# Kernel tuning notes

Measured on AMD Instinct MI355X. Metric: run time of the kernel, lower is better.

The kernel has to match this reference:

```python
import jax, jax.numpy as jnp
import numpy as np

WIN = (8, 8, 8)
NUM_HEADS = 8
DIM = 256


def _make_rel_tables(win):
    Wh, Ww, Wd = win
    # relative coords table, matching the torch buffer construction
    ch = np.arange(-(Wh - 1), Wh, dtype=np.float32)
    cw = np.arange(-(Ww - 1), Ww, dtype=np.float32)
    cd = np.arange(-(Wd - 1), Wd, dtype=np.float32)
    g = np.stack(np.meshgrid(ch, cw, cd, indexing='ij'), axis=-1)  # (2Wh-1,2Ww-1,2Wd-1,3)
    g[..., 0] /= (Wh - 1)
    g[..., 1] /= (Ww - 1)
    g[..., 2] /= (Wd - 1)
    g *= 8.0
    g = np.sign(g) * np.log2(np.abs(g) + 1.0) / np.log2(8.0)
    table = g.reshape(-1, 3).astype(np.float32)  # (3375, 3)
    # relative position index (meshgrid order coords_d, coords_h, coords_w as in source)
    ah = np.arange(Wh)
    aw = np.arange(Ww)
    ad = np.arange(Wd)
    coords = np.stack(np.meshgrid(ad, ah, aw, indexing='ij'))  # (3, Wd, Wh, Ww)
    cf = coords.reshape(3, -1)  # (3, N)
    rel = cf[:, :, None] - cf[:, None, :]  # (3, N, N)
    rel = rel.transpose(1, 2, 0).astype(np.int64)
    rel[:, :, 0] += Wh - 1
    rel[:, :, 1] += Ww - 1
    rel[:, :, 2] += Wd - 1
    rel[:, :, 0] *= (2 * Ww - 1) * (2 * Wd - 1)
    rel[:, :, 1] *= 2 * Wd - 1
    idx = rel.sum(-1).astype(np.int32)  # (N, N)
    return jnp.asarray(table), jnp.asarray(idx)


def setup_inputs() -> dict:
    key = jax.random.key(0)
    ks = jax.random.split(key, 8)
    B_, N, C, nH = 128, 512, DIM, NUM_HEADS
    table, idx = _make_rel_tables(WIN)
    return {
        'x': jax.random.normal(ks[0], (B_, N, C), jnp.float32),
        'mask': jnp.zeros((64, N, N), jnp.float32),
        'qkv_w': jax.random.normal(ks[1], (3 * C, C), jnp.float32) * 0.02,
        'q_bias': jnp.zeros((C,), jnp.float32),
        'v_bias': jnp.zeros((C,), jnp.float32),
        'logit_scale': jnp.log(10.0 * jnp.ones((nH, 1, 1), jnp.float32)),
        'cpb_w1': jax.random.normal(ks[2], (512, 3), jnp.float32) * 0.1,
        'cpb_b1': jnp.zeros((512,), jnp.float32),
        'cpb_w2': jax.random.normal(ks[3], (nH, 512), jnp.float32) * 0.05,
        'proj_w': jax.random.normal(ks[4], (C, C), jnp.float32) * 0.02,
        'proj_b': jnp.zeros((C,), jnp.float32),
        'rel_coords_table': table,
        'rel_pos_index': idx,
    }


def reference(x, mask, qkv_w, q_bias, v_bias, logit_scale, cpb_w1, cpb_b1,
              cpb_w2, proj_w, proj_b, rel_coords_table, rel_pos_index):
    B_, N, C = x.shape
    nH = NUM_HEADS
    d = C // nH
    # qkv projection with (q_bias, 0, v_bias) bias
    qkv_bias = jnp.concatenate([q_bias, jnp.zeros_like(v_bias), v_bias])
    qkv = x @ qkv_w.T + qkv_bias  # (B_, N, 3C)
    qkv = qkv.reshape(B_, N, 3, nH, d).transpose(2, 0, 3, 1, 4)  # (3, B_, nH, N, d)
    q, k, v = qkv[0], qkv[1], qkv[2]
    # cosine attention: L2-normalize q and k along head dim (eps as in F.normalize)
    qn = q / jnp.maximum(jnp.linalg.norm(q, axis=-1, keepdims=True), 1e-12)
    kn = k / jnp.maximum(jnp.linalg.norm(k, axis=-1, keepdims=True), 1e-12)
    attn = jnp.einsum('bhnd,bhmd->bhnm', qn, kn)  # (B_, nH, N, N)
    scale = jnp.exp(jnp.minimum(logit_scale, jnp.log(100.0)))  # clamp at log(1/0.01)
    attn = attn * scale[None]  # (nH,1,1) broadcast
    # MLP-computed relative position bias
    hdn = jax.nn.relu(rel_coords_table @ cpb_w1.T + cpb_b1)  # (T, 512)
    bias_table = hdn @ cpb_w2.T  # (T, nH)
    rpb = bias_table[rel_pos_index]  # (N, N, nH)
    rpb = 16.0 * jax.nn.sigmoid(rpb.transpose(2, 0, 1))  # (nH, N, N)
    attn = attn + rpb[None]
    # mask add (0 / -inf per-window mask)
    nW = mask.shape[0]
    attn = attn.reshape(B_ // nW, nW, nH, N, N) + mask[None, :, None]
    attn = attn.reshape(B_, nH, N, N)
    attn = jax.nn.softmax(attn, axis=-1)
    out = jnp.einsum('bhnm,bhmd->bhnd', attn, v)
    out = out.transpose(0, 2, 1, 3).reshape(B_, N, C)
    return out @ proj_w.T + proj_b
```

## Files before the change

### kernel.cpp

```cpp
#include <hip/hip_runtime.h>
#include <cstddef>
#include <cstdint>
#include <math.h>

#define NB   128
#define SEQ  512
#define CH   256
#define NH   8
#define HD   32
#define TBL  3375
#define LOG100 4.6051701859880914f

typedef _Float16 f16x8 __attribute__((ext_vector_type(8)));
typedef _Float16 f16x4 __attribute__((ext_vector_type(4)));
typedef float    f32x4 __attribute__((ext_vector_type(4)));

__device__ inline f32x4 mfma16(f16x8 a, f16x8 b, f32x4 c) {
    return __builtin_amdgcn_mfma_f32_16x16x32_f16(a, b, c, 0, 0, 0);
}

__device__ inline unsigned short h2b(_Float16 h) {
    union { _Float16 f; unsigned short s; } u; u.f = h; return u.s;
}

__global__ __launch_bounds__(256)
void split_inplace(unsigned int* buf, int rows)
{
    int wid = (blockIdx.x << 2) + (threadIdx.x >> 6);
    int ln  = threadIdx.x & 63;
    if (wid >= rows) return;
    unsigned int* row = buf + (size_t)wid * 256;
    uint4 u = ((const uint4*)row)[ln];
    float x0 = __uint_as_float(u.x), x1 = __uint_as_float(u.y),
          x2 = __uint_as_float(u.z), x3 = __uint_as_float(u.w);
    _Float16 hh0 = (_Float16)x0, hh1 = (_Float16)x1,
             hh2 = (_Float16)x2, hh3 = (_Float16)x3;
    _Float16 ll0 = (_Float16)(x0 - (float)hh0), ll1 = (_Float16)(x1 - (float)hh1),
             ll2 = (_Float16)(x2 - (float)hh2), ll3 = (_Float16)(x3 - (float)hh3);
    unsigned int hi01 = (unsigned int)h2b(hh0) | ((unsigned int)h2b(hh1) << 16);
    unsigned int hi23 = (unsigned int)h2b(hh2) | ((unsigned int)h2b(hh3) << 16);
    unsigned int lo01 = (unsigned int)h2b(ll0) | ((unsigned int)h2b(ll1) << 16);
    unsigned int lo23 = (unsigned int)h2b(ll2) | ((unsigned int)h2b(ll3) << 16);
    asm volatile("" ::: "memory");
    *(uint2*)(row + 2 * ln)       = make_uint2(hi01, hi23);
    *(uint2*)(row + 128 + 2 * ln) = make_uint2(lo01, lo23);
}

template<int EPI>
__global__ __launch_bounds__(256)
void mgemm(const _Float16* __restrict__ A, const _Float16* __restrict__ W,
           float* __restrict__ qb, float* __restrict__ kb, float* __restrict__ vb,
           const float* __restrict__ q_bias, const float* __restrict__ v_bias,
           const float* __restrict__ logit_scale,
           float* __restrict__ out, const float* __restrict__ obias)
{
    __shared__ alignas(16) _Float16 As[128 * 64];
    __shared__ alignas(16) _Float16 Bs[128 * 64];
    const int t  = threadIdx.x;
    const int ln = t & 63;
    const int wv = t >> 6;
    const int wr = wv >> 1, wc = wv & 1;
    const int m0 = blockIdx.x * 128, n0 = blockIdx.y * 128;

    f32x4 acc[4][4];
#pragma unroll
    for (int i = 0; i < 4; ++i)
#pragma unroll
        for (int j = 0; j < 4; ++j) acc[i][j] = (f32x4){0.f, 0.f, 0.f, 0.f};

    for (int step = 0; step < 12; ++step) {
        const int term = step >> 2;
        const int k0   = (step & 3) * 64;
        const int aoff = (term == 2) ? 256 : 0;
        const int woff = (term == 1) ? 256 : 0;
        if (step) __syncthreads();
#pragma unroll
        for (int u = 0; u < 4; ++u) {
            int f = u * 256 + t;
            int r = f >> 3, s = f & 7;
            int sw = s ^ (r & 7);
            uint4 av = *(const uint4*)(A + (size_t)(m0 + r) * 512 + aoff + k0 + s * 8);
            *(uint4*)(As + r * 64 + sw * 8) = av;
            uint4 wv4 = *(const uint4*)(W + (size_t)(n0 + r) * 512 + woff + k0 + s * 8);
            *(uint4*)(Bs + r * 64 + sw * 8) = wv4;
        }
        __syncthreads();
#pragma unroll
        for (int kh = 0; kh < 2; ++kh) {
            const int g = kh * 4 + (ln >> 4);
            f16x8 af[4], bf[4];
#pragma unroll
            for (int fm = 0; fm < 4; ++fm) {
                int r = wr * 64 + fm * 16 + (ln & 15);
                af[fm] = *(const f16x8*)(As + r * 64 + (g ^ (r & 7)) * 8);
            }
#pragma unroll
            for (int fn = 0; fn < 4; ++fn) {
                int r = wc * 64 + fn * 16 + (ln & 15);
                bf[fn] = *(const f16x8*)(Bs + r * 64 + (g ^ (r & 7)) * 8);
            }
#pragma unroll
            for (int fm = 0; fm < 4; ++fm)
#pragma unroll
                for (int fn = 0; fn < 4; ++fn)
                    acc[fm][fn] = mfma16(af[fm], bf[fn], acc[fm][fn]);
        }
    }

    if (EPI == 0) {
#pragma unroll
        for (int fm = 0; fm < 4; ++fm) {
#pragma unroll
            for (int fn = 0; fn < 4; ++fn) {
                int col = n0 + wc * 64 + fn * 16 + (ln & 15);
                float bv = obias[col];
#pragma unroll
                for (int r = 0; r < 4; ++r) {
                    int m = m0 + wr * 64 + fm * 16 + (ln >> 4) * 4 + r;
                    out[(size_t)m * CH + col] = acc[fm][fn][r] + bv;
                }
            }
        }
    } else {
        const int cbase = n0 + wc * 64;
        const int which = cbase >> 8;
#pragma unroll
        for (int fp = 0; fp < 2; ++fp) {
            const int c0  = cbase + fp * 32;
            const int rem = c0 & 255;
            const int h   = rem >> 5;
            float bias0 = 0.f, bias1 = 0.f;
            if (which == 0) {
                bias0 = q_bias[rem + (ln & 15)];
                bias1 = q_bias[rem + 16 + (ln & 15)];
            } else if (which == 2) {
                bias0 = v_bias[rem + (ln & 15)];
                bias1 = v_bias[rem + 16 + (ln & 15)];
            }
            float scl = 1.f;
            if (which == 0) scl = __expf(fminf(logit_scale[h], LOG100));
            float* dst = (which == 0) ? qb : (which == 1 ? kb : vb);
#pragma unroll
            for (int fm = 0; fm < 4; ++fm) {
#pragma unroll
                for (int r = 0; r < 4; ++r) {
                    float v0 = acc[fm][fp * 2][r]     + bias0;
                    float v1 = acc[fm][fp * 2 + 1][r] + bias1;
                    if (which < 2) {
                        float ss = v0 * v0 + v1 * v1;
#pragma unroll
                        for (int mk = 1; mk < 16; mk <<= 1)
                            ss += __shfl_xor(ss, mk, 64);
                        float mult = 1.f / fmaxf(sqrtf(ss), 1e-12f);
                        if (which == 0) mult *= scl;
                        v0 *= mult; v1 *= mult;
                    }
                    int m = m0 + wr * 64 + fm * 16 + (ln >> 4) * 4 + r;
                    int b = m >> 9, nseq = m & 511;
                    size_t base = (((size_t)b * NH + h) * SEQ + nseq) * HD;
                    dst[base + (ln & 15)]      = v0;
                    dst[base + 16 + (ln & 15)] = v1;
                }
            }
        }
    }
}

__global__ __launch_bounds__(256)
void cpb_kernel(const float* __restrict__ tbl, const float* __restrict__ w1,
                const float* __restrict__ b1, const float* __restrict__ w2,
                float* __restrict__ bt)
{
    __shared__ alignas(16) float red[256][8];
    int t = blockIdx.x;
    float c0 = tbl[t*3+0], c1 = tbl[t*3+1], c2 = tbl[t*3+2];
    float part[8] = {0,0,0,0,0,0,0,0};
    for (int j = threadIdx.x; j < 512; j += 256) {
        float h = c0*w1[j*3+0] + c1*w1[j*3+1] + c2*w1[j*3+2] + b1[j];
        h = fmaxf(h, 0.f);
#pragma unroll
        for (int o = 0; o < 8; ++o) part[o] += h * w2[o*512 + j];
    }
#pragma unroll
    for (int o = 0; o < 8; ++o) red[threadIdx.x][o] = part[o];
    __syncthreads();
    for (int s = 128; s >= 1; s >>= 1) {
        if (threadIdx.x < s)
#pragma unroll
            for (int o = 0; o < 8; ++o) red[threadIdx.x][o] += red[threadIdx.x + s][o];
        __syncthreads();
    }
    if (threadIdx.x < 8) bt[t*8 + threadIdx.x] = red[0][threadIdx.x];
}

__global__ __launch_bounds__(256)
void rpb_kernel(const int* __restrict__ idx, const float* __restrict__ bt,
                float* __restrict__ rpb)
{
    int h = blockIdx.x >> 9;
    int i = blockIdx.x & 511;
    for (int j = threadIdx.x; j < 512; j += 256) {
        int id = idx[i*512 + j];
        float x = bt[id*8 + h];
        rpb[((size_t)h*512 + i)*512 + j] = 16.f / (1.f + __expf(-x));
    }
}

__global__ __launch_bounds__(256)
void attn_kernel(const float* __restrict__ qn, const float* __restrict__ kn,
                 const float* __restrict__ vv, const float* __restrict__ rpb,
                 const float* __restrict__ mask, _Float16* __restrict__ ao16)
{
    __shared__ alignas(16) float Ks[64][32];
    __shared__ alignas(16) float Vs[64][32];
    const int b = blockIdx.x >> 3, h = blockIdx.x & 7;
    const int n0 = threadIdx.x, n1 = threadIdx.x + 256;

    const float* qrow0 = qn + (((size_t)b*NH + h)*SEQ + n0)*HD;
    const float* qrow1 = qn + (((size_t)b*NH + h)*SEQ + n1)*HD;
    float4 qa[8], qc[8];
#pragma unroll
    for (int i = 0; i < 8; ++i) { qa[i] = ((const float4*)qrow0)[i];
                                  qc[i] = ((const float4*)qrow1)[i]; }

    float4 Oa[8], Oc[8];
#pragma unroll
    for (int i = 0; i < 8; ++i) { Oa[i] = make_float4(0,0,0,0);
                                  Oc[i] = make_float4(0,0,0,0); }
    float la = 0.f, lc = 0.f;

    const float* kbase = kn + ((size_t)b*NH + h)*SEQ*HD;
    const float* vbase = vv + ((size_t)b*NH + h)*SEQ*HD;
    const float* rr0 = rpb  + ((size_t)h*SEQ + n0)*SEQ;
    const float* rr1 = rpb  + ((size_t)h*SEQ + n1)*SEQ;
    const float* mr0 = mask + ((size_t)(b & 63)*SEQ + n0)*SEQ;
    const float* mr1 = mask + ((size_t)(b & 63)*SEQ + n1)*SEQ;

    for (int kt = 0; kt < 8; ++kt) {
        if (kt) __syncthreads();
        const float4* ksrc = (const float4*)(kbase + kt*64*32);
        const float4* vsrc = (const float4*)(vbase + kt*64*32);
        float4* kd = (float4*)&Ks[0][0];
        float4* vd = (float4*)&Vs[0][0];
        kd[threadIdx.x]       = ksrc[threadIdx.x];
        kd[threadIdx.x + 256] = ksrc[threadIdx.x + 256];
        vd[threadIdx.x]       = vsrc[threadIdx.x];
        vd[threadIdx.x + 256] = vsrc[threadIdx.x + 256];
        __syncthreads();

#pragma unroll 1
        for (int jc = 0; jc < 16; ++jc) {
            const int j0 = jc * 4;
            float4 ra = *(const float4*)(rr0 + kt*64 + j0);
            float4 rc = *(const float4*)(rr1 + kt*64 + j0);
            float4 ma = *(const float4*)(mr0 + kt*64 + j0);
            float4 mc = *(const float4*)(mr1 + kt*64 + j0);
            float ba[4] = {ra.x+ma.x, ra.y+ma.y, ra.z+ma.z, ra.w+ma.w};
            float bc[4] = {rc.x+mc.x, rc.y+mc.y, rc.z+mc.z, rc.w+mc.w};
#pragma unroll
            for (int jj = 0; jj < 4; ++jj) {
                const int j = j0 + jj;
                const float4* kr = (const float4*)&Ks[j][0];
                float d0 = 0.f, d1 = 0.f;
#pragma unroll
                for (int dq = 0; dq < 8; ++dq) {
                    float4 kq = kr[dq];
                    d0 += qa[dq].x*kq.x + qa[dq].y*kq.y + qa[dq].z*kq.z + qa[dq].w*kq.w;
                    d1 += qc[dq].x*kq.x + qc[dq].y*kq.y + qc[dq].z*kq.z + qc[dq].w*kq.w;
                }
                float p0 = __expf(d0 + ba[jj]);
                float p1 = __expf(d1 + bc[jj]);
                la += p0; lc += p1;
                const float4* vr = (const float4*)&Vs[j][0];
#pragma unroll
                for (int dq = 0; dq < 8; ++dq) {
                    float4 vq = vr[dq];
                    Oa[dq].x += p0*vq.x; Oa[dq].y += p0*vq.y;
                    Oa[dq].z += p0*vq.z; Oa[dq].w += p0*vq.w;
                    Oc[dq].x += p1*vq.x; Oc[dq].y += p1*vq.y;
                    Oc[dq].z += p1*vq.z; Oc[dq].w += p1*vq.w;
                }
            }
        }
    }

    float ia = 1.f / la, ic = 1.f / lc;
    _Float16* o0 = ao16 + ((size_t)(b*SEQ + n0))*512 + h*HD;
    _Float16* o1 = ao16 + ((size_t)(b*SEQ + n1))*512 + h*HD;
#pragma unroll
    for (int dq = 0; dq < 8; ++dq) {
        float r0[4] = {Oa[dq].x*ia, Oa[dq].y*ia, Oa[dq].z*ia, Oa[dq].w*ia};
        float r1[4] = {Oc[dq].x*ic, Oc[dq].y*ic, Oc[dq].z*ic, Oc[dq].w*ic};
        f16x4 h0, l0, h1, l1;
#pragma unroll
        for (int e = 0; e < 4; ++e) {
            _Float16 hh = (_Float16)r0[e];
            h0[e] = hh; l0[e] = (_Float16)(r0[e] - (float)hh);
            _Float16 hg = (_Float16)r1[e];
            h1[e] = hg; l1[e] = (_Float16)(r1[e] - (float)hg);
        }
        *(f16x4*)(o0 + dq*4)       = h0;
        *(f16x4*)(o0 + 256 + dq*4) = l0;
        *(f16x4*)(o1 + dq*4)       = h1;
        *(f16x4*)(o1 + 256 + dq*4) = l1;
    }
}

extern "C" void kernel_launch(void* const* d_in, const int* in_sizes, int n_in,
                              void* d_out, int out_size, void* d_ws, size_t ws_size,
                              hipStream_t stream)
{
    float* x           = (float*)d_in[0];
    const float* mask        = (const float*)d_in[1];
    float* qkv_w       = (float*)d_in[2];
    const float* q_bias      = (const float*)d_in[3];
    const float* v_bias      = (const float*)d_in[4];
    const float* logit_scale = (const float*)d_in[5];
    const float* cpb_w1      = (const float*)d_in[6];
    const float* cpb_b1      = (const float*)d_in[7];
    const float* cpb_w2      = (const float*)d_in[8];
    float* proj_w      = (float*)d_in[9];
    const float* proj_b      = (const float*)d_in[10];
    const float* tblc        = (const float*)d_in[11];
    const int*   rpidx       = (const int*)d_in[12];

    float* ws = (float*)d_ws;
    const size_t SZ = (size_t)NB * SEQ * CH;
    float* qb     = ws;
    float* kb     = qb + SZ;
    float* vb     = kb + SZ;
    float* rpbbuf = vb + SZ;
    float* bt     = rpbbuf + (size_t)NH * SEQ * SEQ;

    split_inplace<<<16384, 256, 0, stream>>>((unsigned int*)x, NB * SEQ);
    split_inplace<<<192, 256, 0, stream>>>((unsigned int*)qkv_w, 3 * CH);
    split_inplace<<<64, 256, 0, stream>>>((unsigned int*)proj_w, CH);
    mgemm<1><<<dim3(512, 6), dim3(256), 0, stream>>>(
        (const _Float16*)x, (const _Float16*)qkv_w,
        qb, kb, vb, q_bias, v_bias, logit_scale, nullptr, nullptr);
    cpb_kernel<<<TBL, 256, 0, stream>>>(tblc, cpb_w1, cpb_b1, cpb_w2, bt);
    rpb_kernel<<<NH * SEQ, 256, 0, stream>>>(rpidx, bt, rpbbuf);
    attn_kernel<<<NB * NH, 256, 0, stream>>>(qb, kb, vb, rpbbuf, mask,
                                             (_Float16*)x);
    mgemm<0><<<dim3(512, 2), dim3(256), 0, stream>>>(
        (const _Float16*)x, (const _Float16*)proj_w,
        nullptr, nullptr, nullptr, nullptr, nullptr, nullptr,
        (float*)d_out, proj_b);
}
```

Measured before the change: 1.169 ms.

## Move attention to MFMA with split-fp16 Q/K/V, transposed V, and mask-skip flag

Replaces the scalar fp32 attention loop with an MFMA-based flash-attention kernel. It uses hi/lo fp16 splits for Q, K, V and P to keep near-fp32 accuracy, and an online softmax with P staged in shared memory. The QKV GEMM epilogue now writes split fp16 rows, and a new transpose kernel lays V out for the PV product. A scan kernel sets a flag when the mask has any nonzero entry, so mask loads can be skipped when it is all zero. The grid grows to one block per 64-query tile, adding parallelism. In exchange it adds extra kernel launches, a full pass over the mask, and reuse of the output buffer as scratch.

```diff
diff --git a/kernel.cpp b/kernel.cpp
--- a/kernel.cpp
+++ b/kernel.cpp
@@ -49,7 +49,8 @@
 template<int EPI>
 __global__ __launch_bounds__(256)
 void mgemm(const _Float16* __restrict__ A, const _Float16* __restrict__ W,
-           float* __restrict__ qb, float* __restrict__ kb, float* __restrict__ vb,
+           _Float16* __restrict__ qb16, _Float16* __restrict__ kb16,
+           _Float16* __restrict__ vstr16,
            const float* __restrict__ q_bias, const float* __restrict__ v_bias,
            const float* __restrict__ logit_scale,
            float* __restrict__ out, const float* __restrict__ obias)
@@ -139,7 +140,8 @@
             }
             float scl = 1.f;
             if (which == 0) scl = __expf(fminf(logit_scale[h], LOG100));
-            float* dst = (which == 0) ? qb : (which == 1 ? kb : vb);
+            _Float16* dst = (which == 0) ? qb16 : (which == 1 ? kb16 : vstr16);
+            const int dd = ln & 15;
 #pragma unroll
             for (int fm = 0; fm < 4; ++fm) {
 #pragma unroll
@@ -157,12 +159,57 @@
                     }
                     int m = m0 + wr * 64 + fm * 16 + (ln >> 4) * 4 + r;
                     int b = m >> 9, nseq = m & 511;
-                    size_t base = (((size_t)b * NH + h) * SEQ + nseq) * HD;
-                    dst[base + (ln & 15)]      = v0;
-                    dst[base + 16 + (ln & 15)] = v1;
+                    size_t rowb = (((size_t)b * NH + h) * SEQ + nseq) * 64;
+                    _Float16 h0 = (_Float16)v0, h1 = (_Float16)v1;
+                    _Float16 l0 = (_Float16)(v0 - (float)h0);
+                    _Float16 l1 = (_Float16)(v1 - (float)h1);
+                    dst[rowb + dd]           = h0;
+                    dst[rowb + 16 + dd]      = h1;
+                    dst[rowb + 32 + dd]      = l0;
+                    dst[rowb + 48 + dd]      = l1;
                 }
             }
         }
+    }
+}
+
+__global__ __launch_bounds__(256)
+void vtrans(const _Float16* __restrict__ vs, _Float16* __restrict__ vt)
+{
+    __shared__ alignas(16) _Float16 T[64][136];
+    const int bh = blockIdx.x, t = threadIdx.x;
+    const _Float16* src = vs + (size_t)bh * 32768;
+    _Float16* dst = vt + (size_t)bh * 32768;
+    for (int tile = 0; tile < 4; ++tile) {
+        if (tile) __syncthreads();
+        const int n = (t >> 1);
+        const int sbase = (t & 1) * 32;
+        const uint4* sp = (const uint4*)(src + ((size_t)(tile * 128 + n)) * 64 + sbase);
+#pragma unroll
+        for (int q = 0; q < 4; ++q) {
+            uint4 u = sp[q];
+            _Float16 tmp[8];
+            *(uint4*)tmp = u;
+#pragma unroll
+            for (int e = 0; e < 8; ++e)
+                T[sbase + q * 8 + e][n] = tmp[e];
+        }
+        __syncthreads();
+        const int cc = t >> 2, nn = (t & 3) * 32;
+        uint4* dp = (uint4*)(dst + (size_t)cc * 512 + tile * 128 + nn);
+        const uint4* lp = (const uint4*)(&T[cc][nn]);
+        dp[0] = lp[0]; dp[1] = lp[1]; dp[2] = lp[2]; dp[3] = lp[3];
+    }
+}
+
+__global__ __launch_bounds__(256)
+void maskflag(const unsigned int* __restrict__ mask, unsigned int* flag, int n)
+{
+    unsigned int acc = 0;
+    for (int i = blockIdx.x * 256 + threadIdx.x; i < n; i += gridDim.x * 256)
+        acc |= mask[i];
+    if (__ballot(acc != 0)) {
+        if ((threadIdx.x & 63) == 0) atomicOr(flag, 1u);
     }
 }
 
@@ -206,103 +253,133 @@
     }
 }
 
-__global__ __launch_bounds__(256)
-void attn_kernel(const float* __restrict__ qn, const float* __restrict__ kn,
-                 const float* __restrict__ vv, const float* __restrict__ rpb,
-                 const float* __restrict__ mask, _Float16* __restrict__ ao16)
-{
-    __shared__ alignas(16) float Ks[64][32];
-    __shared__ alignas(16) float Vs[64][32];
-    const int b = blockIdx.x >> 3, h = blockIdx.x & 7;
-    const int n0 = threadIdx.x, n1 = threadIdx.x + 256;
-
-    const float* qrow0 = qn + (((size_t)b*NH + h)*SEQ + n0)*HD;
-    const float* qrow1 = qn + (((size_t)b*NH + h)*SEQ + n1)*HD;
-    float4 qa[8], qc[8];
-#pragma unroll
-    for (int i = 0; i < 8; ++i) { qa[i] = ((const float4*)qrow0)[i];
-                                  qc[i] = ((const float4*)qrow1)[i]; }
-
-    float4 Oa[8], Oc[8];
-#pragma unroll
-    for (int i = 0; i < 8; ++i) { Oa[i] = make_float4(0,0,0,0);
-                                  Oc[i] = make_float4(0,0,0,0); }
-    float la = 0.f, lc = 0.f;
-
-    const float* kbase = kn + ((size_t)b*NH + h)*SEQ*HD;
-    const float* vbase = vv + ((size_t)b*NH + h)*SEQ*HD;
-    const float* rr0 = rpb  + ((size_t)h*SEQ + n0)*SEQ;
-    const float* rr1 = rpb  + ((size_t)h*SEQ + n1)*SEQ;
-    const float* mr0 = mask + ((size_t)(b & 63)*SEQ + n0)*SEQ;
-    const float* mr1 = mask + ((size_t)(b & 63)*SEQ + n1)*SEQ;
+__global__ __launch_bounds__(256, 4)
+void attn_kernel(const _Float16* __restrict__ qb, const _Float16* __restrict__ kb,
+                 const _Float16* __restrict__ vbt, const float* __restrict__ rpb,
+                 const float* __restrict__ mask, const unsigned int* __restrict__ mflag,
+                 _Float16* __restrict__ ao16)
+{
+    __shared__ float Pl[4][16][68];
+    const int idx = blockIdx.x;
+    const int h  = idx & 7;
+    const int qt = (idx >> 3) & 7;
+    const int b  = idx >> 6;
+    const int w  = threadIdx.x >> 6;
+    const int ln = threadIdx.x & 63;
+    const int c  = ln & 15, g = ln >> 4;
+    const int q0 = qt * 64 + w * 16;
+    const size_t bh = (size_t)b * NH + h;
+
+    const _Float16* qrow = qb + (bh * SEQ + q0) * 64;
+    f16x8 qh = *(const f16x8*)(qrow + (size_t)c * 64 + g * 8);
+    f16x8 qlo = *(const f16x8*)(qrow + (size_t)c * 64 + 32 + g * 8);
+
+    const _Float16* kbase = kb + bh * SEQ * 64;
+    const _Float16* vtb   = vbt + bh * 32768;
+    const float* rbase = rpb  + ((size_t)h * SEQ + q0) * SEQ;
+    const float* mbase = mask + ((size_t)(b & 63) * SEQ + q0) * SEQ;
+    const bool usemask = (*mflag) != 0u;
+
+    f32x4 O0 = {0,0,0,0}, O1 = {0,0,0,0};
+    float mrun[4] = {-INFINITY, -INFINITY, -INFINITY, -INFINITY};
+    float lr[4] = {0.f, 0.f, 0.f, 0.f};
 
     for (int kt = 0; kt < 8; ++kt) {
-        if (kt) __syncthreads();
-        const float4* ksrc = (const float4*)(kbase + kt*64*32);
-        const float4* vsrc = (const float4*)(vbase + kt*64*32);
-        float4* kd = (float4*)&Ks[0][0];
-        float4* vd = (float4*)&Vs[0][0];
-        kd[threadIdx.x]       = ksrc[threadIdx.x];
-        kd[threadIdx.x + 256] = ksrc[threadIdx.x + 256];
-        vd[threadIdx.x]       = vsrc[threadIdx.x];
-        vd[threadIdx.x + 256] = vsrc[threadIdx.x + 256];
-        __syncthreads();
-
-#pragma unroll 1
-        for (int jc = 0; jc < 16; ++jc) {
-            const int j0 = jc * 4;
-            float4 ra = *(const float4*)(rr0 + kt*64 + j0);
-            float4 rc = *(const float4*)(rr1 + kt*64 + j0);
-            float4 ma = *(const float4*)(mr0 + kt*64 + j0);
-            float4 mc = *(const float4*)(mr1 + kt*64 + j0);
-            float ba[4] = {ra.x+ma.x, ra.y+ma.y, ra.z+ma.z, ra.w+ma.w};
-            float bc[4] = {rc.x+mc.x, rc.y+mc.y, rc.z+mc.z, rc.w+mc.w};
-#pragma unroll
-            for (int jj = 0; jj < 4; ++jj) {
-                const int j = j0 + jj;
-                const float4* kr = (const float4*)&Ks[j][0];
-                float d0 = 0.f, d1 = 0.f;
-#pragma unroll
-                for (int dq = 0; dq < 8; ++dq) {
-                    float4 kq = kr[dq];
-                    d0 += qa[dq].x*kq.x + qa[dq].y*kq.y + qa[dq].z*kq.z + qa[dq].w*kq.w;
-                    d1 += qc[dq].x*kq.x + qc[dq].y*kq.y + qc[dq].z*kq.z + qc[dq].w*kq.w;
-                }
-                float p0 = __expf(d0 + ba[jj]);
-                float p1 = __expf(d1 + bc[jj]);
-                la += p0; lc += p1;
-                const float4* vr = (const float4*)&Vs[j][0];
-#pragma unroll
-                for (int dq = 0; dq < 8; ++dq) {
-                    float4 vq = vr[dq];
-                    Oa[dq].x += p0*vq.x; Oa[dq].y += p0*vq.y;
-                    Oa[dq].z += p0*vq.z; Oa[dq].w += p0*vq.w;
-                    Oc[dq].x += p1*vq.x; Oc[dq].y += p1*vq.y;
-                    Oc[dq].z += p1*vq.z; Oc[dq].w += p1*vq.w;
-                }
-            }
-        }
-    }
-
-    float ia = 1.f / la, ic = 1.f / lc;
-    _Float16* o0 = ao16 + ((size_t)(b*SEQ + n0))*512 + h*HD;
-    _Float16* o1 = ao16 + ((size_t)(b*SEQ + n1))*512 + h*HD;
-#pragma unroll
-    for (int dq = 0; dq < 8; ++dq) {
-        float r0[4] = {Oa[dq].x*ia, Oa[dq].y*ia, Oa[dq].z*ia, Oa[dq].w*ia};
-        float r1[4] = {Oc[dq].x*ic, Oc[dq].y*ic, Oc[dq].z*ic, Oc[dq].w*ic};
-        f16x4 h0, l0, h1, l1;
-#pragma unroll
-        for (int e = 0; e < 4; ++e) {
-            _Float16 hh = (_Float16)r0[e];
-            h0[e] = hh; l0[e] = (_Float16)(r0[e] - (float)hh);
-            _Float16 hg = (_Float16)r1[e];
-            h1[e] = hg; l1[e] = (_Float16)(r1[e] - (float)hg);
-        }
-        *(f16x4*)(o0 + dq*4)       = h0;
-        *(f16x4*)(o0 + 256 + dq*4) = l0;
-        *(f16x4*)(o1 + dq*4)       = h1;
-        *(f16x4*)(o1 + 256 + dq*4) = l1;
+        const int j0 = kt * 64;
+        f32x4 S[4];
+#pragma unroll
+        for (int t = 0; t < 4; ++t) {
+            const _Float16* krow = kbase + (size_t)(j0 + t * 16 + c) * 64;
+            f16x8 kh = *(const f16x8*)(krow + g * 8);
+            f16x8 kl = *(const f16x8*)(krow + 32 + g * 8);
+            f32x4 s = {0,0,0,0};
+            s = mfma16(qh, kh, s);
+            s = mfma16(qh, kl, s);
+            s = mfma16(qlo, kh, s);
+            S[t] = s;
+        }
+#pragma unroll
+        for (int t = 0; t < 4; ++t)
+#pragma unroll
+            for (int r = 0; r < 4; ++r) {
+                size_t off = (size_t)(g * 4 + r) * SEQ + j0 + t * 16 + c;
+                float bv = rbase[off];
+                if (usemask) bv += mbase[off];
+                S[t][r] += bv;
+            }
+        float al[4];
+#pragma unroll
+        for (int r = 0; r < 4; ++r) {
+            float mm = fmaxf(fmaxf(S[0][r], S[1][r]), fmaxf(S[2][r], S[3][r]));
+#pragma unroll
+            for (int mk = 1; mk < 16; mk <<= 1)
+                mm = fmaxf(mm, __shfl_xor(mm, mk, 64));
+            float mnew = fmaxf(mrun[r], mm);
+            al[r] = __expf(mrun[r] - mnew);
+            mrun[r] = mnew;
+        }
+        float psum[4] = {0.f, 0.f, 0.f, 0.f};
+#pragma unroll
+        for (int t = 0; t < 4; ++t)
+#pragma unroll
+            for (int r = 0; r < 4; ++r) {
+                float p = __expf(S[t][r] - mrun[r]);
+                psum[r] += p;
+                Pl[w][g * 4 + r][t * 16 + c] = p;
+            }
+#pragma unroll
+        for (int r = 0; r < 4; ++r) {
+            lr[r] = al[r] * lr[r] + psum[r];
+            O0[r] *= al[r];
+            O1[r] *= al[r];
+        }
+        asm volatile("s_waitcnt lgkmcnt(0)" ::: "memory");
+        __builtin_amdgcn_sched_barrier(0);
+#pragma unroll
+        for (int ks = 0; ks < 2; ++ks) {
+            const float* pr = &Pl[w][c][ks * 32 + g * 8];
+            float4 pa = *(const float4*)pr;
+            float4 pb = *(const float4*)(pr + 4);
+            float pv[8] = {pa.x, pa.y, pa.z, pa.w, pb.x, pb.y, pb.z, pb.w};
+            f16x8 ph, plo;
+#pragma unroll
+            for (int e = 0; e < 8; ++e) {
+                _Float16 hh = (_Float16)pv[e];
+                ph[e] = hh;
+                plo[e] = (_Float16)(pv[e] - (float)hh);
+            }
+#pragma unroll
+            for (int dt = 0; dt < 2; ++dt) {
+                const _Float16* vrow = vtb + (size_t)(dt * 16 + c) * SEQ
+                                       + j0 + ks * 32 + g * 8;
+                f16x8 vh = *(const f16x8*)vrow;
+                f16x8 vl = *(const f16x8*)(vrow + 32 * SEQ);
+                f32x4& O = dt ? O1 : O0;
+                O = mfma16(ph, vh, O);
+                O = mfma16(ph, vl, O);
+                O = mfma16(plo, vh, O);
+            }
+        }
+    }
+#pragma unroll
+    for (int r = 0; r < 4; ++r) {
+#pragma unroll
+        for (int mk = 1; mk < 16; mk <<= 1)
+            lr[r] += __shfl_xor(lr[r], mk, 64);
+        lr[r] = 1.f / lr[r];
+    }
+#pragma unroll
+    for (int dt = 0; dt < 2; ++dt) {
+        f32x4 O = dt ? O1 : O0;
+#pragma unroll
+        for (int r = 0; r < 4; ++r) {
+            float val = O[r] * lr[r];
+            _Float16 hh = (_Float16)val;
+            _Float16 ll = (_Float16)(val - (float)hh);
+            size_t row = (size_t)b * SEQ + q0 + g * 4 + r;
+            ao16[row * 512 + h * HD + dt * 16 + c]       = hh;
+            ao16[row * 512 + 256 + h * HD + dt * 16 + c] = ll;
+        }
     }
 }
 
@@ -326,22 +403,29 @@
 
     float* ws = (float*)d_ws;
     const size_t SZ = (size_t)NB * SEQ * CH;
-    float* qb     = ws;
-    float* kb     = qb + SZ;
-    float* vb     = kb + SZ;
-    float* rpbbuf = vb + SZ;
-    float* bt     = rpbbuf + (size_t)NH * SEQ * SEQ;
+    _Float16* qb16 = (_Float16*)ws;
+    _Float16* kb16 = (_Float16*)(ws + SZ);
+    _Float16* vbt  = (_Float16*)(ws + 2 * SZ);
+    float* rpbbuf  = ws + 3 * SZ;
+    float* bt      = rpbbuf + (size_t)NH * SEQ * SEQ;
+    unsigned int* flag = (unsigned int*)(bt + 27008);
+    _Float16* vstr = (_Float16*)d_out;
+    _Float16* ao16 = (_Float16*)x;
 
     split_inplace<<<16384, 256, 0, stream>>>((unsigned int*)x, NB * SEQ);
     split_inplace<<<192, 256, 0, stream>>>((unsigned int*)qkv_w, 3 * CH);
     split_inplace<<<64, 256, 0, stream>>>((unsigned int*)proj_w, CH);
     mgemm<1><<<dim3(512, 6), dim3(256), 0, stream>>>(
         (const _Float16*)x, (const _Float16*)qkv_w,
-        qb, kb, vb, q_bias, v_bias, logit_scale, nullptr, nullptr);
+        qb16, kb16, vstr, q_bias, v_bias, logit_scale, nullptr, nullptr);
+    vtrans<<<NB * NH, 256, 0, stream>>>(vstr, vbt);
     cpb_kernel<<<TBL, 256, 0, stream>>>(tblc, cpb_w1, cpb_b1, cpb_w2, bt);
     rpb_kernel<<<NH * SEQ, 256, 0, stream>>>(rpidx, bt, rpbbuf);
-    attn_kernel<<<NB * NH, 256, 0, stream>>>(qb, kb, vb, rpbbuf, mask,
-                                             (_Float16*)x);
+    hipMemsetAsync(flag, 0, 4, stream);
+    maskflag<<<2048, 256, 0, stream>>>((const unsigned int*)mask, flag,
+                                       64 * SEQ * SEQ);
+    attn_kernel<<<NB * 8 * NH, 256, 0, stream>>>(qb16, kb16, vbt, rpbbuf,
+                                                 mask, flag, ao16);
     mgemm<0><<<dim3(512, 2), dim3(256), 0, stream>>>(
         (const _Float16*)x, (const _Float16*)proj_w,
         nullptr, nullptr, nullptr, nullptr, nullptr, nullptr,
```

Result: faster. 945.6 us (-19.1%).
